# Kernel tuning notes

Hardware: AMD Instinct MI355X
Metric: run time of the kernel (lower is better)

The kernel has to match this reference:

```python
import jax, jax.numpy as jnp
import numpy as np

DIM = 96
HEADS = 6
WS = 8                      # window_size
OWS = int(WS * 0.5) + WS    # overlap_win_size = 12
PAD = (OWS - WS) // 2       # 2
Dd = Hh = Ww = 24
B = 1
L = Dd * Hh * Ww
MLP_H = DIM * 2
TBL = (WS + OWS - 1) ** 3   # 6859 relative-position-bias entries


def setup_inputs() -> dict:
    key = jax.random.key(0)
    ks = jax.random.split(key, 8)
    def n(k, shape, s=0.02):
        return jax.random.normal(k, shape, jnp.float32) * s
    return {
        "x": jax.random.normal(ks[0], (B, L, DIM), jnp.float32),
        "ln1_w": jnp.ones((DIM,), jnp.float32),
        "ln1_b": jnp.zeros((DIM,), jnp.float32),
        "qkv_w": n(ks[1], (3 * DIM, DIM)),
        "qkv_b": jnp.zeros((3 * DIM,), jnp.float32),
        "rpb": n(ks[2], (TBL, HEADS)),
        "proj_w": n(ks[3], (DIM, DIM)),
        "proj_b": jnp.zeros((DIM,), jnp.float32),
        "ln2_w": jnp.ones((DIM,), jnp.float32),
        "ln2_b": jnp.zeros((DIM,), jnp.float32),
        "fc1_w": n(ks[4], (MLP_H, DIM)),
        "fc1_b": jnp.zeros((MLP_H,), jnp.float32),
        "fc2_w": n(ks[5], (DIM, MLP_H)),
        "fc2_b": jnp.zeros((DIM,), jnp.float32),
        "rpi": jax.random.randint(ks[6], (WS ** 3, OWS ** 3), 0, TBL),
        "D": Dd, "H": Hh, "W": Ww,
    }


def _ln(x, w, b):
    m = jnp.mean(x, -1, keepdims=True)
    v = jnp.var(x, -1, keepdims=True)
    return (x - m) / jnp.sqrt(v + 1e-5) * w + b


def _ocab3d(x, ln1_w, ln1_b, qkv_w, qkv_b, rpb, proj_w, proj_b,
            ln2_w, ln2_b, fc1_w, fc1_b, fc2_w, fc2_b, rpi, D, H, W):
    Bz, Lz, C = x.shape
    hd = C // HEADS
    scale = hd ** -0.5
    shortcut = x

    xn = _ln(x, ln1_w, ln1_b).reshape(Bz, D, H, W, C)
    qkv = xn @ qkv_w.T + qkv_b                   # [B,D,H,W,3C]
    q = qkv[..., :C]
    kv = qkv[..., C:]                            # cat(k, v) on channels, [B,D,H,W,2C]

    nD, nH, nW = D // WS, H // WS, W // WS
    nw = nD * nH * nW

    # non-overlapping query windows -> [B*nw, WS^3, C]
    qw = q.reshape(Bz, nD, WS, nH, WS, nW, WS, C)
    qw = qw.transpose(0, 1, 3, 5, 2, 4, 6, 7).reshape(Bz * nw, WS ** 3, C)

    # overlapping kv windows via pad + strided gather (mirrors F.pad + unfold)
    kvp = jnp.pad(kv, ((0, 0), (PAD, PAD), (PAD, PAD), (PAD, PAD), (0, 0)))
    idx_d = (jnp.arange(nD) * WS)[:, None] + jnp.arange(OWS)[None, :]
    idx_h = (jnp.arange(nH) * WS)[:, None] + jnp.arange(OWS)[None, :]
    idx_w = (jnp.arange(nW) * WS)[:, None] + jnp.arange(OWS)[None, :]
    kw = kvp[:, idx_d]                 # [B,nD,OWS,Hp,Wp,2C]
    kw = kw[:, :, :, idx_h]            # [B,nD,OWS,nH,OWS,Wp,2C]
    kw = kw[:, :, :, :, :, idx_w]      # [B,nD,OWS,nH,OWS,nW,OWS,2C]
    kw = kw.transpose(0, 1, 3, 5, 2, 4, 6, 7).reshape(Bz * nw, OWS ** 3, 2 * C)
    kk, vv = kw[..., :C], kw[..., C:]

    qh = qw.reshape(-1, WS ** 3, HEADS, hd).transpose(0, 2, 1, 3) * scale
    kh = kk.reshape(-1, OWS ** 3, HEADS, hd).transpose(0, 2, 1, 3)
    vh = vv.reshape(-1, OWS ** 3, HEADS, hd).transpose(0, 2, 1, 3)

    attn = jnp.einsum('bhqd,bhkd->bhqk', qh, kh)               # [B*nw,H,512,1728]
    bias = rpb[rpi.reshape(-1)].reshape(WS ** 3, OWS ** 3, HEADS).transpose(2, 0, 1)
    attn = jax.nn.softmax(attn + bias[None], axis=-1)
    out = jnp.einsum('bhqk,bhkd->bhqd', attn, vh)
    out = out.transpose(0, 2, 1, 3).reshape(Bz * nw, WS ** 3, C)

    # window reverse -> [B, L, C]
    out = out.reshape(Bz, nD, nH, nW, WS, WS, WS, C)
    out = out.transpose(0, 1, 4, 2, 5, 3, 6, 7).reshape(Bz, D * H * W, C)

    x2 = out @ proj_w.T + proj_b + shortcut
    h1 = jax.nn.gelu(_ln(x2, ln2_w, ln2_b) @ fc1_w.T + fc1_b, approximate=False)
    return x2 + (h1 @ fc2_w.T + fc2_b)


def reference(x, ln1_w, ln1_b, qkv_w, qkv_b, rpb, proj_w, proj_b,
              ln2_w, ln2_b, fc1_w, fc1_b, fc2_w, fc2_b, rpi, D, H, W):
    return _ocab3d(x, ln1_w, ln1_b, qkv_w, qkv_b, rpb, proj_w, proj_b,
                   ln2_w, ln2_b, fc1_w, fc1_b, fc2_w, fc2_b, rpi, D, H, W)
```

## Files before the change

kernel.cpp:

```cpp
#include <hip/hip_runtime.h>
#include <math.h>

#define DIMC   96
#define NHEADS 6
#define HD     16
#define WSZ    8
#define OWSZ   12
#define PADW   2
#define DD     24
#define LTOK   13824
#define NWIN   27
#define NKEY   1728
#define NROW   512
#define MLPH   192
#define PDIM   28
#define PD3    21952
#define TBL    6859
#define LSTR   82944
#define AOSTR  1327104
#define LOG2E  1.4426950408889634f

typedef __attribute__((ext_vector_type(4))) short bf16x4;
typedef __attribute__((ext_vector_type(8))) short bf16x8;
typedef __attribute__((ext_vector_type(4))) float f32x4;

__device__ __forceinline__ unsigned short bfround(float f) {
    unsigned u = __float_as_uint(f);
    return (unsigned short)((u + 0x7FFFu + ((u >> 16) & 1u)) >> 16);
}
__device__ __forceinline__ unsigned bfpack(float a, float b) {
    unsigned ua = __float_as_uint(a), ub = __float_as_uint(b);
    ua = (ua + 0x7FFFu + ((ua >> 16) & 1u)) >> 16;
    ub = (ub + 0x7FFFu + ((ub >> 16) & 1u)) >> 16;
    return ua | (ub << 16);
}
__device__ __forceinline__ uint4 pack8(const float* v) {
    uint4 u;
    u.x = bfpack(v[0], v[1]); u.y = bfpack(v[2], v[3]);
    u.z = bfpack(v[4], v[5]); u.w = bfpack(v[6], v[7]);
    return u;
}
__device__ __forceinline__ bf16x4 pack4(f32x4 p) {
    union { uint2 u; bf16x4 v; } r;
    r.u.x = __builtin_amdgcn_perm(__float_as_uint(p[1]), __float_as_uint(p[0]), 0x07060302u);
    r.u.y = __builtin_amdgcn_perm(__float_as_uint(p[3]), __float_as_uint(p[2]), 0x07060302u);
    return r.v;
}
__device__ __forceinline__ f32x4 cvt4(uint2 b) {
    f32x4 c;
    c[0] = __uint_as_float(b.x << 16);
    c[1] = __uint_as_float(b.x & 0xffff0000u);
    c[2] = __uint_as_float(b.y << 16);
    c[3] = __uint_as_float(b.y & 0xffff0000u);
    return c;
}
__device__ __forceinline__ f32x4 mfma16(bf16x4 a, bf16x4 b, f32x4 c) {
#if __has_builtin(__builtin_amdgcn_mfma_f32_16x16x16bf16_1k)
    return __builtin_amdgcn_mfma_f32_16x16x16bf16_1k(a, b, c, 0, 0, 0);
#else
    bf16x8 a8 = {a[0], a[1], a[2], a[3], 0, 0, 0, 0};
    bf16x8 b8 = {b[0], b[1], b[2], b[3], 0, 0, 0, 0};
    return __builtin_amdgcn_mfma_f32_16x16x32_bf16(a8, b8, c, 0, 0, 0);
#endif
}
__device__ __forceinline__ f32x4 mfma32k(bf16x8 a, bf16x8 b, f32x4 c) {
    return __builtin_amdgcn_mfma_f32_16x16x32_bf16(a, b, c, 0, 0, 0);
}
__device__ __forceinline__ float fexp2(float x) {
#if __has_builtin(__builtin_amdgcn_exp2f)
    return __builtin_amdgcn_exp2f(x);
#else
    return exp2f(x);
#endif
}

#define QKVB 1296
#define ZB   515
#define WPB  45
#define BIASB 216
__global__ __launch_bounds__(256) void qkvz_kernel(
        const float* __restrict__ X, const float* __restrict__ W,
        const float* __restrict__ bias, const float* __restrict__ lnw,
        const float* __restrict__ lnb,
        const float* __restrict__ projw, const float* __restrict__ fc1w,
        const float* __restrict__ fc2w,
        const int* __restrict__ rpi, const float* __restrict__ rpb,
        unsigned short* __restrict__ q16, unsigned short* __restrict__ kvp2,
        uint4* __restrict__ wpack, unsigned short* __restrict__ biasP) {
    __shared__ uint4 Af4[2 * 3 * 4 * 16];
    __shared__ uint4 Bf4[6 * 3 * 4 * 16];
    int bx = blockIdx.x, tid = threadIdx.x;

    if (bx >= QKVB + ZB + WPB) {
        int b2 = bx - (QKVB + ZB + WPB);
        int g = b2 >> 1, qh = b2 & 1;
        int qi = qh * 256 + tid;
        const int* rp = rpi + (long)qi * NKEY + (g >> 2) * 64
                        + ((g >> 1) & 1) * 32 + (g & 1) * 4;
        #pragma unroll
        for (int quadj = 0; quadj < 4; ++quadj) {
            int4 t = *(const int4*)(rp + quadj * 8);
            const float2* p0 = (const float2*)(rpb + (long)t.x * 6);
            const float2* p1 = (const float2*)(rpb + (long)t.y * 6);
            const float2* p2 = (const float2*)(rpb + (long)t.z * 6);
            const float2* p3 = (const float2*)(rpb + (long)t.w * 6);
            unsigned short* oq = biasP + ((long)(g * 4 + quadj) * 512 + qi) * 4;
            #pragma unroll
            for (int hp = 0; hp < 3; ++hp) {
                float2 a0 = p0[hp], a1 = p1[hp], a2 = p2[hp], a3 = p3[hp];
                uint2 ua, ub;
                ua.x = bfpack(a0.x * LOG2E, a1.x * LOG2E);
                ua.y = bfpack(a2.x * LOG2E, a3.x * LOG2E);
                ub.x = bfpack(a0.y * LOG2E, a1.y * LOG2E);
                ub.y = bfpack(a2.y * LOG2E, a3.y * LOG2E);
                *(uint2*)(oq + (long)(hp * 2)     * 884736) = ua;
                *(uint2*)(oq + (long)(hp * 2 + 1) * 884736) = ub;
            }
        }
        return;
    }
    if (bx >= QKVB + ZB) {
        int u = (bx - QKVB - ZB) * 256 + tid;
        if (u < 5760) {
            int p = (u < 1152) ? u : (u < 3456 ? (u - 1152) % 1152 : (u - 3456) % 1152);
            int nn = p & 15, r = p >> 4, qg = r & 3, r2 = r >> 2;
            int kt = r2 % 3, ct = r2 / 3;
            int n = ct * 16 + nn, g = kt * 4 + qg;
            const float* src;
            if (u < 1152)      src = projw + n * 96 + g * 8;
            else if (u < 3456) { int nc = (u - 1152) / 1152; src = fc1w + (long)(nc * 96 + n) * 96 + g * 8; }
            else               { int kh = (u - 3456) / 1152; src = fc2w + (long)n * 192 + kh * 96 + g * 8; }
            const float4* s4 = (const float4*)src;
            float v[8];
            float4 t0 = s4[0], t1 = s4[1];
            v[0]=t0.x; v[1]=t0.y; v[2]=t0.z; v[3]=t0.w;
            v[4]=t1.x; v[5]=t1.y; v[6]=t1.z; v[7]=t1.w;
            wpack[u] = pack8(v);
        }
        return;
    }
    if (bx >= QKVB) {
        int t = (bx - QKVB) * 256 + tid;
        if (t < 21952 * 6) {
            int head = t / PD3, pos = t % PD3;
            int d = pos / 784, h = (pos / 28) % 28, w = pos % 28;
            if (d < 2 || d >= 26 || h < 2 || h >= 26 || w < 2 || w >= 26) {
                uint4* p = (uint4*)(kvp2 + ((long)head * PD3 + pos) * 32);
                uint4 z = make_uint4(0, 0, 0, 0);
                p[0] = z; p[1] = z; p[2] = z; p[3] = z;
            }
        }
        return;
    }

    int nc   = bx % 3;
    int row0 = (bx / 3) * 32;

    if (tid < 128) {
        int row = tid >> 2, part = tid & 3;
        int rt = row >> 4, mm = row & 15;
        float v[24];
        const float4* xp = (const float4*)(X + (long)(row0 + row) * 96 + part * 24);
        float s = 0.f, sq = 0.f;
        #pragma unroll
        for (int i = 0; i < 6; ++i) {
            float4 t = xp[i];
            v[i*4+0] = t.x; v[i*4+1] = t.y; v[i*4+2] = t.z; v[i*4+3] = t.w;
            s  += t.x + t.y + t.z + t.w;
            sq += t.x*t.x + t.y*t.y + t.z*t.z + t.w*t.w;
        }
        s  += __shfl_xor(s, 1);  s  += __shfl_xor(s, 2);
        sq += __shfl_xor(sq, 1); sq += __shfl_xor(sq, 2);
        float mean = s * (1.f / 96.f);
        float inv  = rsqrtf(sq * (1.f / 96.f) - mean * mean + 1e-5f);
        const float4* wp = (const float4*)(lnw + part * 24);
        const float4* bp = (const float4*)(lnb + part * 24);
        #pragma unroll
        for (int i = 0; i < 6; ++i) {
            float4 wv = wp[i], bv = bp[i];
            v[i*4+0] = (v[i*4+0] - mean) * inv * wv.x + bv.x;
            v[i*4+1] = (v[i*4+1] - mean) * inv * wv.y + bv.y;
            v[i*4+2] = (v[i*4+2] - mean) * inv * wv.z + bv.z;
            v[i*4+3] = (v[i*4+3] - mean) * inv * wv.w + bv.w;
        }
        #pragma unroll
        for (int gg = 0; gg < 3; ++gg) {
            int g = part * 3 + gg;
            int kt = g >> 2, qq = g & 3;
            Af4[((rt * 3 + kt) * 4 + qq) * 16 + mm] = pack8(v + gg * 8);
        }
    }
    for (int idx = tid; idx < 96 * 12; idx += 256) {
        int n = idx / 12;
        int g = idx % 12;
        const float4* wp = (const float4*)(W + (long)(nc * 96 + n) * 96 + g * 8);
        float v[8];
        float4 t0 = wp[0], t1 = wp[1];
        v[0]=t0.x; v[1]=t0.y; v[2]=t0.z; v[3]=t0.w;
        v[4]=t1.x; v[5]=t1.y; v[6]=t1.z; v[7]=t1.w;
        int ct = n >> 4, nn = n & 15, kt = g >> 2, qg = g & 3;
        Bf4[((ct * 3 + kt) * 4 + qg) * 16 + nn] = pack8(v);
    }
    __syncthreads();

    int wave = tid >> 6, lane = tid & 63;
    int qq = lane >> 4, mI = lane & 15;
    int rt = wave & 1, cg = wave >> 1;

    f32x4 acc[3];
    #pragma unroll
    for (int j = 0; j < 3; ++j) acc[j] = (f32x4){0.f, 0.f, 0.f, 0.f};
    #pragma unroll
    for (int kt = 0; kt < 3; ++kt) {
        bf16x8 a = *(const bf16x8*)&Af4[((rt * 3 + kt) * 4 + qq) * 16 + mI];
        #pragma unroll
        for (int j = 0; j < 3; ++j) {
            bf16x8 b = *(const bf16x8*)&Bf4[(((cg * 3 + j) * 3 + kt) * 4 + qq) * 16 + mI];
            acc[j] = __builtin_amdgcn_mfma_f32_16x16x32_bf16(a, b, acc[j], 0, 0, 0);
        }
    }

    float bv[3];
    #pragma unroll
    for (int j = 0; j < 3; ++j) bv[j] = bias[nc * 96 + (cg * 3 + j) * 16 + mI];
    #pragma unroll
    for (int r = 0; r < 4; ++r) {
        int row = row0 + rt * 16 + qq * 4 + r;
        if (nc == 0) {
            unsigned short* op = q16 + (long)row * 96;
            #pragma unroll
            for (int j = 0; j < 3; ++j)
                op[(cg * 3 + j) * 16 + mI] = bfround(0.25f * LOG2E * (acc[j][r] + bv[j]));
        } else {
            int d = row / 576, hh = (row / 24) % 24, w2 = row % 24;
            long pos = ((long)(d + 2) * 28 + (hh + 2)) * 28 + (w2 + 2);
            #pragma unroll
            for (int j = 0; j < 3; ++j) {
                int head = cg * 3 + j;
                kvp2[((long)head * PD3 + pos) * 32 +
                     (nc == 2 ? 16 : 0) + mI] = bfround(acc[j][r] + bv[j]);
            }
        }
    }
}

#define KSTR 20
#define VST2 22

#define ATTN_STEP(P, BCUR, BNXT)                                              \
    {                                                                         \
        int c = c0 + cc + (P);                                                \
        bool more = (cc + (P) + 1 < cn);                                      \
        if (more) stgn = *kvaddr(c + 1);                                      \
        __syncthreads();                                                      \
        bf16x4 kf[4];                                                         \
        kf[0] = *(const bf16x4*)&Ks[(P)][kfO];                                \
        kf[1] = *(const bf16x4*)&Ks[(P)][kfO + 4 * KSTR];                     \
        kf[2] = *(const bf16x4*)&Ks[(P)][kfO + 32 * KSTR];                    \
        kf[3] = *(const bf16x4*)&Ks[(P)][kfO + 36 * KSTR];                    \
        f32x4 S[2][4];                                                        \
        _Pragma("unroll")                                                     \
        for (int qt = 0; qt < 2; ++qt) {                                      \
            _Pragma("unroll")                                                 \
            for (int kt = 0; kt < 4; ++kt)                                    \
                S[qt][kt] = mfma16(kf[kt], qf[qt], cvt4(BCUR[qt][kt]));       \
        }                                                                     \
        if (more) {                                                           \
            const unsigned short* bp = bbase + (long)(c + 1) * 32768;         \
            _Pragma("unroll")                                                 \
            for (int qt = 0; qt < 2; ++qt) {                                  \
                _Pragma("unroll")                                             \
                for (int kt = 0; kt < 4; ++kt)                                \
                    BNXT[qt][kt] = *(const uint2*)(bp + kt * 8192 + qt * 64); \
            }                                                                 \
        }                                                                     \
        bf16x8 P8[2][2];                                                      \
        _Pragma("unroll")                                                     \
        for (int qt = 0; qt < 2; ++qt) {                                      \
            _Pragma("unroll")                                                 \
            for (int u = 0; u < 2; ++u) {                                     \
                f32x4 p0, p1;                                                 \
                _Pragma("unroll")                                             \
                for (int r = 0; r < 4; ++r) {                                 \
                    p0[r] = fexp2(S[qt][2 * u][r]);                           \
                    p1[r] = fexp2(S[qt][2 * u + 1][r]);                       \
                }                                                             \
                union { struct { bf16x4 lo, hi; } h; bf16x8 v; } uu;          \
                uu.h.lo = pack4(p0); uu.h.hi = pack4(p1);                     \
                P8[qt][u] = uu.v;                                             \
                lacc[qt] = mfma32k(P8[qt][u], ones8, lacc[qt]);               \
            }                                                                 \
        }                                                                     \
        _Pragma("unroll")                                                     \
        for (int u = 0; u < 2; ++u) {                                         \
            union { unsigned short s[8]; bf16x8 v; } vb;                      \
            int vbase = (u * 32 + quad * 8) * VST2 + m16;                     \
            _Pragma("unroll")                                                 \
            for (int i = 0; i < 8; ++i) vb.s[i] = Vs[(P)][vbase + i * VST2];  \
            o[0] = mfma32k(P8[0][u], vb.v, o[0]);                             \
            o[1] = mfma32k(P8[1][u], vb.v, o[1]);                             \
        }                                                                     \
        if (more) writeLDS((P) ^ 1, stgn);                                    \
    }

__global__ __launch_bounds__(256, 3) void attn_kernel(
        const unsigned short* __restrict__ q, const unsigned short* __restrict__ kvp2,
        const unsigned short* __restrict__ biasP, float* __restrict__ ao,
        float* __restrict__ lbuf) {
    __shared__ unsigned short Ks[2][64 * KSTR];
    __shared__ unsigned short Vs[2][64 * VST2];
    int bid = blockIdx.x;
    int w = bid / 48, rem = bid % 48;
    int head = rem >> 3;
    int quart = (rem >> 1) & 3, half = rem & 1;
    int wd8 = (w / 9) * 8, wh8 = ((w / 3) % 3) * 8, ww8 = (w % 3) * 8;
    int tid = threadIdx.x, wave = tid >> 6, lane = tid & 63;
    int quad = lane >> 4, m16 = lane & 15;
    int key = tid >> 2, part = tid & 3;
    int c0 = half ? 13 : 0;
    int cn = half ? 14 : 13;

    auto kvaddr = [&](int c) -> const uint4* {
        int jg = c * 64 + key;
        int i = jg / 144, jh = (jg / 12) % 12, jw = jg % 12;
        long sp = ((long)(wd8 + i) * PDIM + (wh8 + jh)) * PDIM + (ww8 + jw);
        return (const uint4*)(kvp2 + ((long)head * PD3 + sp) * 32 + part * 8);
    };
    auto writeLDS = [&](int b, uint4 v) {
        if (part < 2) {
            *(uint2*)(&Ks[b][key * KSTR + part * 8])     = make_uint2(v.x, v.y);
            *(uint2*)(&Ks[b][key * KSTR + part * 8 + 4]) = make_uint2(v.z, v.w);
        } else {
            int d0 = (part - 2) * 8;
            *(uint2*)(&Vs[b][key * VST2 + d0])     = make_uint2(v.x, v.y);
            *(uint2*)(&Vs[b][key * VST2 + d0 + 4]) = make_uint2(v.z, v.w);
        }
    };

    bf16x4 qf[2];
    #pragma unroll
    for (int qt = 0; qt < 2; ++qt) {
        int ql = quart * 128 + wave * 32 + qt * 16 + m16;
        int ld = ql >> 6, lh = (ql >> 3) & 7, lw = ql & 7;
        int g = ((wd8 + ld) * 24 + (wh8 + lh)) * 24 + (ww8 + lw);
        qf[qt] = *(const bf16x4*)(q + (long)g * 96 + head * 16 + quad * 4);
    }

    const unsigned short* bbase = biasP + (long)head * 884736 + quad * 2048
                         + ((quart * 128 + wave * 32 + m16) << 2);
    uint2 bb0[2][4], bb1[2][4];
    #pragma unroll
    for (int qt = 0; qt < 2; ++qt)
        #pragma unroll
        for (int kt = 0; kt < 4; ++kt)
            bb0[qt][kt] = *(const uint2*)(bbase + (long)(c0 * 4 + kt) * 8192 + qt * 64);

    writeLDS(0, *kvaddr(c0));

    int kfO = ((m16 >> 2) * 8 + (m16 & 3)) * KSTR + quad * 4;

    const bf16x8 ones8 = {(short)0x3F80, (short)0x3F80, (short)0x3F80, (short)0x3F80,
                          (short)0x3F80, (short)0x3F80, (short)0x3F80, (short)0x3F80};
    f32x4 o[2], lacc[2];
    o[0] = (f32x4){0.f,0.f,0.f,0.f}; o[1] = (f32x4){0.f,0.f,0.f,0.f};
    lacc[0] = o[0]; lacc[1] = o[1];
    uint4 stgn;

    for (int cc = 0; cc < cn; cc += 2) {
        ATTN_STEP(0, bb0, bb1)
        if (cc + 1 < cn) ATTN_STEP(1, bb1, bb0)
    }

    float* aout = ao + (long)half * AOSTR;
    float* lout = lbuf + (long)half * LSTR;
    #pragma unroll
    for (int qt = 0; qt < 2; ++qt) {
        #pragma unroll
        for (int r = 0; r < 4; ++r) {
            int ql = quart * 128 + wave * 32 + qt * 16 + quad * 4 + r;
            int ld = ql >> 6, lh = (ql >> 3) & 7, lw = ql & 7;
            int g = ((wd8 + ld) * 24 + (wh8 + lh)) * 24 + (ww8 + lw);
            aout[(long)g * 96 + head * 16 + m16] = o[qt][r];
            if (m16 == 0) lout[g * 6 + head] = lacc[qt][r];
        }
    }
}

#define X2S 100
__global__ __launch_bounds__(512) void mlp_kernel(
        const float* __restrict__ ao0, const float* __restrict__ ao1,
        const float* __restrict__ lbuf, const uint4* __restrict__ wpack,
        const float* __restrict__ projb, const float* __restrict__ x,
        const float* __restrict__ ln2w, const float* __restrict__ ln2b,
        const float* __restrict__ fc1b, const float* __restrict__ fc2b,
        float* __restrict__ out) {
    __shared__ uint4 Ws[5760];
    __shared__ uint4 Af4[4 * 3 * 4 * 16];
    __shared__ float x2s[64 * X2S];
    __shared__ unsigned short h16[64 * 192];
    int tid = threadIdx.x;
    int row0 = blockIdx.x * 64;
    int wave = tid >> 6, lane = tid & 63;
    int qq = lane >> 4, mI = lane & 15;
    int rt = wave & 3, cg = wave >> 2;

    for (int idx = tid; idx < 5760; idx += 512) Ws[idx] = wpack[idx];

    if (tid < 256) {
        int row = tid >> 2, part = tid & 3;
        int rtA = row >> 4, mm = row & 15;
        int grow = row0 + row;
        const float4* a0 = (const float4*)(ao0 + (long)grow * 96 + part * 24);
        const float4* a1 = (const float4*)(ao1 + (long)grow * 96 + part * 24);
        int ha = (part * 3) >> 1, hb = ha + 1;
        float inva = 1.f / (lbuf[grow*6 + ha] + lbuf[LSTR + grow*6 + ha]);
        float invb = 1.f / (lbuf[grow*6 + hb] + lbuf[LSTR + grow*6 + hb]);
        float v[24];
        #pragma unroll
        for (int i = 0; i < 6; ++i) {
            float4 u0 = a0[i], u1 = a1[i];
            #pragma unroll
            for (int j = 0; j < 4; ++j) {
                int gc = part * 24 + i * 4 + j;
                float lv = ((gc >> 4) == ha) ? inva : invb;
                float s = (j==0?u0.x+u1.x : j==1?u0.y+u1.y : j==2?u0.z+u1.z : u0.w+u1.w);
                v[i*4+j] = s * lv;
            }
        }
        #pragma unroll
        for (int gg = 0; gg < 3; ++gg) {
            int g = part * 3 + gg;
            int kt = g >> 2, q4 = g & 3;
            Af4[((rtA * 3 + kt) * 4 + q4) * 16 + mm] = pack8(v + gg * 8);
        }
    }
    __syncthreads();

    {
        f32x4 acc[3];
        #pragma unroll
        for (int j = 0; j < 3; ++j) acc[j] = (f32x4){0.f,0.f,0.f,0.f};
        #pragma unroll
        for (int kt = 0; kt < 3; ++kt) {
            bf16x8 a = *(const bf16x8*)&Af4[((rt * 3 + kt) * 4 + qq) * 16 + mI];
            #pragma unroll
            for (int j = 0; j < 3; ++j) {
                bf16x8 b = *(const bf16x8*)&Ws[(((cg * 3 + j) * 3 + kt) * 4 + qq) * 16 + mI];
                acc[j] = __builtin_amdgcn_mfma_f32_16x16x32_bf16(a, b, acc[j], 0, 0, 0);
            }
        }
        float bv[3];
        #pragma unroll
        for (int j = 0; j < 3; ++j) bv[j] = projb[(cg * 3 + j) * 16 + mI];
        #pragma unroll
        for (int r = 0; r < 4; ++r) {
            int row = rt * 16 + qq * 4 + r;
            int grow = row0 + row;
            #pragma unroll
            for (int j = 0; j < 3; ++j) {
                int col = (cg * 3 + j) * 16 + mI;
                x2s[row * X2S + col] = acc[j][r] + bv[j] + x[(long)grow * 96 + col];
            }
        }
    }
    __syncthreads();

    if (tid < 256) {
        int row = tid >> 2, part = tid & 3;
        int rtA = row >> 4, mm = row & 15;
        float v[24];
        const float4* xp = (const float4*)(x2s + row * X2S + part * 24);
        float s = 0.f, sq = 0.f;
        #pragma unroll
        for (int i = 0; i < 6; ++i) {
            float4 t = xp[i];
            v[i*4+0] = t.x; v[i*4+1] = t.y; v[i*4+2] = t.z; v[i*4+3] = t.w;
            s  += t.x + t.y + t.z + t.w;
            sq += t.x*t.x + t.y*t.y + t.z*t.z + t.w*t.w;
        }
        s  += __shfl_xor(s, 1);  s  += __shfl_xor(s, 2);
        sq += __shfl_xor(sq, 1); sq += __shfl_xor(sq, 2);
        float mean = s * (1.f / 96.f);
        float inv  = rsqrtf(sq * (1.f / 96.f) - mean * mean + 1e-5f);
        const float4* wp = (const float4*)(ln2w + part * 24);
        const float4* bp = (const float4*)(ln2b + part * 24);
        #pragma unroll
        for (int i = 0; i < 6; ++i) {
            float4 wv = wp[i], bv = bp[i];
            v[i*4+0] = (v[i*4+0] - mean) * inv * wv.x + bv.x;
            v[i*4+1] = (v[i*4+1] - mean) * inv * wv.y + bv.y;
            v[i*4+2] = (v[i*4+2] - mean) * inv * wv.z + bv.z;
            v[i*4+3] = (v[i*4+3] - mean) * inv * wv.w + bv.w;
        }
        #pragma unroll
        for (int gg = 0; gg < 3; ++gg) {
            int g = part * 3 + gg;
            int kt = g >> 2, q4 = g & 3;
            Af4[((rtA * 3 + kt) * 4 + q4) * 16 + mm] = pack8(v + gg * 8);
        }
    }
    __syncthreads();

    #pragma unroll
    for (int nc = 0; nc < 2; ++nc) {
        f32x4 acc[3];
        #pragma unroll
        for (int j = 0; j < 3; ++j) acc[j] = (f32x4){0.f,0.f,0.f,0.f};
        #pragma unroll
        for (int kt = 0; kt < 3; ++kt) {
            bf16x8 a = *(const bf16x8*)&Af4[((rt * 3 + kt) * 4 + qq) * 16 + mI];
            #pragma unroll
            for (int j = 0; j < 3; ++j) {
                bf16x8 b = *(const bf16x8*)&Ws[1152 + nc * 1152 +
                               (((cg * 3 + j) * 3 + kt) * 4 + qq) * 16 + mI];
                acc[j] = __builtin_amdgcn_mfma_f32_16x16x32_bf16(a, b, acc[j], 0, 0, 0);
            }
        }
        float bv[3];
        #pragma unroll
        for (int j = 0; j < 3; ++j) bv[j] = fc1b[nc * 96 + (cg * 3 + j) * 16 + mI];
        #pragma unroll
        for (int r = 0; r < 4; ++r) {
            int row = rt * 16 + qq * 4 + r;
            #pragma unroll
            for (int j = 0; j < 3; ++j) {
                int col = nc * 96 + (cg * 3 + j) * 16 + mI;
                float v = acc[j][r] + bv[j];
                float g = 0.5f * v * (1.f + erff(v * 0.70710678f));
                int fi = (((row >> 4) * 6 + (col >> 5)) * 4 + ((col >> 3) & 3)) * 16 + (row & 15);
                h16[fi * 8 + (col & 7)] = bfround(g);
            }
        }
    }
    __syncthreads();

    f32x4 acc2[3];
    #pragma unroll
    for (int j = 0; j < 3; ++j) acc2[j] = (f32x4){0.f,0.f,0.f,0.f};
    #pragma unroll
    for (int kh = 0; kh < 2; ++kh) {
        #pragma unroll
        for (int kt = 0; kt < 3; ++kt) {
            int ktA = kh * 3 + kt;
            bf16x8 a = *(const bf16x8*)&h16[(((rt * 6 + ktA) * 4 + qq) * 16 + mI) * 8];
            #pragma unroll
            for (int j = 0; j < 3; ++j) {
                bf16x8 b = *(const bf16x8*)&Ws[3456 + kh * 1152 +
                               (((cg * 3 + j) * 3 + kt) * 4 + qq) * 16 + mI];
                acc2[j] = __builtin_amdgcn_mfma_f32_16x16x32_bf16(a, b, acc2[j], 0, 0, 0);
            }
        }
    }
    float bv[3];
    #pragma unroll
    for (int j = 0; j < 3; ++j) bv[j] = fc2b[(cg * 3 + j) * 16 + mI];
    #pragma unroll
    for (int r = 0; r < 4; ++r) {
        int row = rt * 16 + qq * 4 + r;
        int grow = row0 + row;
        #pragma unroll
        for (int j = 0; j < 3; ++j) {
            int col = (cg * 3 + j) * 16 + mI;
            out[(long)grow * 96 + col] = acc2[j][r] + bv[j] + x2s[row * X2S + col];
        }
    }
}

extern "C" void kernel_launch(void* const* d_in, const int* in_sizes, int n_in,
                              void* d_out, int out_size, void* d_ws, size_t ws_size,
                              hipStream_t stream) {
    const float* x     = (const float*)d_in[0];
    const float* ln1w  = (const float*)d_in[1];
    const float* ln1b  = (const float*)d_in[2];
    const float* qkvw  = (const float*)d_in[3];
    const float* qkvb  = (const float*)d_in[4];
    const float* rpb   = (const float*)d_in[5];
    const float* projw = (const float*)d_in[6];
    const float* projb = (const float*)d_in[7];
    const float* ln2w  = (const float*)d_in[8];
    const float* ln2b  = (const float*)d_in[9];
    const float* fc1w  = (const float*)d_in[10];
    const float* fc1b  = (const float*)d_in[11];
    const float* fc2w  = (const float*)d_in[12];
    const float* fc2b  = (const float*)d_in[13];
    const int*   rpi   = (const int*)d_in[14];
    float* outp = (float*)d_out;

    float* ws = (float*)d_ws;
    float*          aop    = ws;
    unsigned short* q16    = (unsigned short*)(ws + 2654208);
    unsigned short* kvp16  = (unsigned short*)(ws + 3317760);
    unsigned short* biasPh = (unsigned short*)(ws + 5425152);
    float*          lbuf   = ws + 10733568;
    uint4*          wpack  = (uint4*)(ws + 10899456);

    qkvz_kernel<<<QKVB + ZB + WPB + BIASB, 256, 0, stream>>>(
        x, qkvw, qkvb, ln1w, ln1b, projw, fc1w, fc2w, rpi, rpb,
        q16, kvp16, wpack, biasPh);
    attn_kernel<<<NWIN * NHEADS * 4 * 2, 256, 0, stream>>>(q16, kvp16, biasPh, aop, lbuf);
    mlp_kernel<<<LTOK / 64, 512, 0, stream>>>(aop, aop + AOSTR, lbuf, wpack, projb, x,
                                              ln2w, ln2b, fc1b, fc2b, outp);
}
```

Measured before the change: 162.5 us.

## Stage attention bias tiles into LDS via async global-to-LDS loads

```diff
diff --git a/kernel.cpp b/kernel.cpp
--- a/kernel.cpp
+++ b/kernel.cpp
@@ -73,6 +73,15 @@
     return exp2f(x);
 #endif
 }
+__device__ __forceinline__ void gload16(const unsigned short* g, unsigned short* l, int lane) {
+#if __has_builtin(__builtin_amdgcn_global_load_lds)
+    __builtin_amdgcn_global_load_lds(
+        (const __attribute__((address_space(1))) void*)g,
+        (__attribute__((address_space(3))) void*)l, 16, 0, 0);
+#else
+    *((uint4*)l + lane) = *(const uint4*)(g + (long)lane * 8);
+#endif
+}
 
 #define QKVB 1296
 #define ZB   515
@@ -93,18 +102,21 @@
 
     if (bx >= QKVB + ZB + WPB) {
         int b2 = bx - (QKVB + ZB + WPB);
-        int g = b2 >> 1, qh = b2 & 1;
-        int qi = qh * 256 + tid;
-        const int* rp = rpi + (long)qi * NKEY + (g >> 2) * 64
-                        + ((g >> 1) & 1) * 32 + (g & 1) * 4;
-        #pragma unroll
-        for (int quadj = 0; quadj < 4; ++quadj) {
-            int4 t = *(const int4*)(rp + quadj * 8);
+        int c  = b2 % 27;
+        int qp = b2 / 27;
+        int quart = qp >> 1, qt = qp & 1;
+        int wavep = tid >> 6, m16p = tid & 15, quadp = (tid >> 4) & 3;
+        int q = quart * 128 + wavep * 32 + qt * 16 + m16p;
+        const int* rp = rpi + (long)q * NKEY + c * 64 + quadp * 8;
+        long obase = (long)quart * 221184 + c * 8192 + qt * 4096 + tid * 4;
+        #pragma unroll
+        for (int kt = 0; kt < 4; ++kt) {
+            int4 t = *(const int4*)(rp + (kt >> 1) * 32 + (kt & 1) * 4);
             const float2* p0 = (const float2*)(rpb + (long)t.x * 6);
             const float2* p1 = (const float2*)(rpb + (long)t.y * 6);
             const float2* p2 = (const float2*)(rpb + (long)t.z * 6);
             const float2* p3 = (const float2*)(rpb + (long)t.w * 6);
-            unsigned short* oq = biasP + ((long)(g * 4 + quadj) * 512 + qi) * 4;
+            unsigned short* oq = biasP + obase + kt * 1024;
             #pragma unroll
             for (int hp = 0; hp < 3; ++hp) {
                 float2 a0 = p0[hp], a1 = p1[hp], a2 = p2[hp], a3 = p3[hp];
@@ -113,7 +125,7 @@
                 ua.y = bfpack(a2.x * LOG2E, a3.x * LOG2E);
                 ub.x = bfpack(a0.y * LOG2E, a1.y * LOG2E);
                 ub.y = bfpack(a2.y * LOG2E, a3.y * LOG2E);
-                *(uint2*)(oq + (long)(hp * 2)     * 884736) = ua;
+                *(uint2*)(oq + (long)(hp * 2) * 884736)     = ua;
                 *(uint2*)(oq + (long)(hp * 2 + 1) * 884736) = ub;
             }
         }
@@ -244,46 +256,42 @@
     }
 }
 
-#define KSTR 20
 #define VST2 22
 
-#define ATTN_STEP(P, BCUR, BNXT)                                              \
+#define ATTN_STEP(P)                                                          \
     {                                                                         \
         int c = c0 + cc + (P);                                                \
         bool more = (cc + (P) + 1 < cn);                                      \
-        if (more) stgn = *kvaddr(c + 1);                                      \
         __syncthreads();                                                      \
+        if (more) {                                                           \
+            const unsigned short* bsrc = btile + (long)(c + 1) * 8192;        \
+            _Pragma("unroll")                                                 \
+            for (int i = 0; i < 4; ++i)                                       \
+                gload16(bsrc + ((i * 4 + wave) * 64 + lane) * 8,              \
+                        &biasL[(P) ^ 1][(i * 4 + wave) * 512], lane);         \
+            stgn = *kvaddr(c + 1);                                            \
+        }                                                                     \
         bf16x4 kf[4];                                                         \
         kf[0] = *(const bf16x4*)&Ks[(P)][kfO];                                \
-        kf[1] = *(const bf16x4*)&Ks[(P)][kfO + 4 * KSTR];                     \
-        kf[2] = *(const bf16x4*)&Ks[(P)][kfO + 32 * KSTR];                    \
-        kf[3] = *(const bf16x4*)&Ks[(P)][kfO + 36 * KSTR];                    \
-        f32x4 S[2][4];                                                        \
-        _Pragma("unroll")                                                     \
-        for (int qt = 0; qt < 2; ++qt) {                                      \
-            _Pragma("unroll")                                                 \
-            for (int kt = 0; kt < 4; ++kt)                                    \
-                S[qt][kt] = mfma16(kf[kt], qf[qt], cvt4(BCUR[qt][kt]));       \
-        }                                                                     \
-        if (more) {                                                           \
-            const unsigned short* bp = bbase + (long)(c + 1) * 32768;         \
-            _Pragma("unroll")                                                 \
-            for (int qt = 0; qt < 2; ++qt) {                                  \
-                _Pragma("unroll")                                             \
-                for (int kt = 0; kt < 4; ++kt)                                \
-                    BNXT[qt][kt] = *(const uint2*)(bp + kt * 8192 + qt * 64); \
-            }                                                                 \
-        }                                                                     \
+        kf[1] = *(const bf16x4*)&Ks[(P)][kfO + 64];                           \
+        kf[2] = *(const bf16x4*)&Ks[(P)][kfO + 512];                          \
+        kf[3] = *(const bf16x4*)&Ks[(P)][kfO + 576];                          \
         bf16x8 P8[2][2];                                                      \
         _Pragma("unroll")                                                     \
         for (int qt = 0; qt < 2; ++qt) {                                      \
+            f32x4 S[4];                                                       \
+            _Pragma("unroll")                                                 \
+            for (int kt = 0; kt < 4; ++kt) {                                  \
+                uint2 bb = *(const uint2*)&biasL[(P)][(qt * 4 + kt) * 1024 + tid * 4]; \
+                S[kt] = mfma16(kf[kt], qf[qt], cvt4(bb));                     \
+            }                                                                 \
             _Pragma("unroll")                                                 \
             for (int u = 0; u < 2; ++u) {                                     \
                 f32x4 p0, p1;                                                 \
                 _Pragma("unroll")                                             \
                 for (int r = 0; r < 4; ++r) {                                 \
-                    p0[r] = fexp2(S[qt][2 * u][r]);                           \
-                    p1[r] = fexp2(S[qt][2 * u + 1][r]);                       \
+                    p0[r] = fexp2(S[2 * u][r]);                               \
+                    p1[r] = fexp2(S[2 * u + 1][r]);                           \
                 }                                                             \
                 union { struct { bf16x4 lo, hi; } h; bf16x8 v; } uu;          \
                 uu.h.lo = pack4(p0); uu.h.hi = pack4(p1);                     \
@@ -307,8 +315,9 @@
         const unsigned short* __restrict__ q, const unsigned short* __restrict__ kvp2,
         const unsigned short* __restrict__ biasP, float* __restrict__ ao,
         float* __restrict__ lbuf) {
-    __shared__ unsigned short Ks[2][64 * KSTR];
+    __shared__ unsigned short Ks[2][64 * 16];
     __shared__ unsigned short Vs[2][64 * VST2];
+    __shared__ unsigned short biasL[2][8192];
     int bid = blockIdx.x;
     int w = bid / 48, rem = bid % 48;
     int head = rem >> 3;
@@ -328,8 +337,10 @@
     };
     auto writeLDS = [&](int b, uint4 v) {
         if (part < 2) {
-            *(uint2*)(&Ks[b][key * KSTR + part * 8])     = make_uint2(v.x, v.y);
-            *(uint2*)(&Ks[b][key * KSTR + part * 8 + 4]) = make_uint2(v.z, v.w);
+            int swz0 = ((2 * part)     ^ (key & 3)) * 4;
+            int swz1 = ((2 * part + 1) ^ (key & 3)) * 4;
+            *(uint2*)(&Ks[b][key * 16 + swz0]) = make_uint2(v.x, v.y);
+            *(uint2*)(&Ks[b][key * 16 + swz1]) = make_uint2(v.z, v.w);
         } else {
             int d0 = (part - 2) * 8;
             *(uint2*)(&Vs[b][key * VST2 + d0])     = make_uint2(v.x, v.y);
@@ -346,18 +357,18 @@
         qf[qt] = *(const bf16x4*)(q + (long)g * 96 + head * 16 + quad * 4);
     }
 
-    const unsigned short* bbase = biasP + (long)head * 884736 + quad * 2048
-                         + ((quart * 128 + wave * 32 + m16) << 2);
-    uint2 bb0[2][4], bb1[2][4];
-    #pragma unroll
-    for (int qt = 0; qt < 2; ++qt)
-        #pragma unroll
-        for (int kt = 0; kt < 4; ++kt)
-            bb0[qt][kt] = *(const uint2*)(bbase + (long)(c0 * 4 + kt) * 8192 + qt * 64);
-
-    writeLDS(0, *kvaddr(c0));
-
-    int kfO = ((m16 >> 2) * 8 + (m16 & 3)) * KSTR + quad * 4;
+    const unsigned short* btile = biasP + (long)head * 884736 + (long)quart * 221184;
+
+    {
+        const unsigned short* bsrc = btile + (long)c0 * 8192;
+        #pragma unroll
+        for (int i = 0; i < 4; ++i)
+            gload16(bsrc + ((i * 4 + wave) * 64 + lane) * 8,
+                    &biasL[0][(i * 4 + wave) * 512], lane);
+        writeLDS(0, *kvaddr(c0));
+    }
+
+    int kfO = ((m16 >> 2) * 8 + (m16 & 3)) * 16 + ((quad ^ (m16 & 3)) * 4);
 
     const bf16x8 ones8 = {(short)0x3F80, (short)0x3F80, (short)0x3F80, (short)0x3F80,
                           (short)0x3F80, (short)0x3F80, (short)0x3F80, (short)0x3F80};
@@ -366,9 +377,10 @@
     lacc[0] = o[0]; lacc[1] = o[1];
     uint4 stgn;
 
+    #pragma unroll 1
     for (int cc = 0; cc < cn; cc += 2) {
-        ATTN_STEP(0, bb0, bb1)
-        if (cc + 1 < cn) ATTN_STEP(1, bb1, bb0)
+        ATTN_STEP(0)
+        if (cc + 1 < cn) ATTN_STEP(1)
     }
 
     float* aout = ao + (long)half * AOSTR;
```

After: 171.4 us. 1.05x slower.

## Relayout bias buffer per thread and transpose V in LDS for vector reads

Applied to the files above, without the earlier changes.

```diff
diff --git a/kernel.cpp b/kernel.cpp
--- a/kernel.cpp
+++ b/kernel.cpp
@@ -93,18 +93,19 @@
 
     if (bx >= QKVB + ZB + WPB) {
         int b2 = bx - (QKVB + ZB + WPB);
-        int g = b2 >> 1, qh = b2 & 1;
-        int qi = qh * 256 + tid;
-        const int* rp = rpi + (long)qi * NKEY + (g >> 2) * 64
-                        + ((g >> 1) & 1) * 32 + (g & 1) * 4;
-        #pragma unroll
-        for (int quadj = 0; quadj < 4; ++quadj) {
-            int4 t = *(const int4*)(rp + quadj * 8);
+        int c  = b2 % 27;
+        int qp = b2 / 27;
+        int quart = qp >> 1, qt = qp & 1;
+        int wavep = tid >> 6, quadp = (tid >> 4) & 3, m16p = tid & 15;
+        int q = quart * 128 + wavep * 32 + qt * 16 + m16p;
+        const int* rp = rpi + (long)q * NKEY + c * 64 + quadp * 8;
+        #pragma unroll
+        for (int kt = 0; kt < 4; ++kt) {
+            int4 t = *(const int4*)(rp + (kt >> 1) * 32 + (kt & 1) * 4);
             const float2* p0 = (const float2*)(rpb + (long)t.x * 6);
             const float2* p1 = (const float2*)(rpb + (long)t.y * 6);
             const float2* p2 = (const float2*)(rpb + (long)t.z * 6);
             const float2* p3 = (const float2*)(rpb + (long)t.w * 6);
-            unsigned short* oq = biasP + ((long)(g * 4 + quadj) * 512 + qi) * 4;
             #pragma unroll
             for (int hp = 0; hp < 3; ++hp) {
                 float2 a0 = p0[hp], a1 = p1[hp], a2 = p2[hp], a3 = p3[hp];
@@ -113,8 +114,10 @@
                 ua.y = bfpack(a2.x * LOG2E, a3.x * LOG2E);
                 ub.x = bfpack(a0.y * LOG2E, a1.y * LOG2E);
                 ub.y = bfpack(a2.y * LOG2E, a3.y * LOG2E);
-                *(uint2*)(oq + (long)(hp * 2)     * 884736) = ua;
-                *(uint2*)(oq + (long)(hp * 2 + 1) * 884736) = ub;
+                *(uint2*)(biasP + ((long)((2*hp)   * 4 + quart) * 27 + c) * 8192
+                          + qt * 4096 + tid * 16 + kt * 4) = ua;
+                *(uint2*)(biasP + ((long)((2*hp+1) * 4 + quart) * 27 + c) * 8192
+                          + qt * 4096 + tid * 16 + kt * 4) = ub;
             }
         }
         return;
@@ -245,33 +248,37 @@
 }
 
 #define KSTR 20
-#define VST2 22
+#define VKP  66
 
 #define ATTN_STEP(P, BCUR, BNXT)                                              \
     {                                                                         \
-        int c = c0 + cc + (P);                                                \
         bool more = (cc + (P) + 1 < cn);                                      \
-        if (more) stgn = *kvaddr(c + 1);                                      \
+        if (more) stgn = *kvaddr(c0 + cc + (P) + 1);                          \
         __syncthreads();                                                      \
         bf16x4 kf[4];                                                         \
-        kf[0] = *(const bf16x4*)&Ks[(P)][kfO];                                \
-        kf[1] = *(const bf16x4*)&Ks[(P)][kfO + 4 * KSTR];                     \
-        kf[2] = *(const bf16x4*)&Ks[(P)][kfO + 32 * KSTR];                    \
-        kf[3] = *(const bf16x4*)&Ks[(P)][kfO + 36 * KSTR];                    \
+        _Pragma("unroll")                                                     \
+        for (int kt = 0; kt < 4; ++kt)                                        \
+            kf[kt] = *(const bf16x4*)&Ks[(P)][(kt * 16 + m16) * KSTR + quad * 4]; \
+        bf16x8 vb0 = *(const bf16x8*)&Vt[(P)][m16 * VKP + quad * 8];          \
+        bf16x8 vb1 = *(const bf16x8*)&Vt[(P)][m16 * VKP + 32 + quad * 8];     \
         f32x4 S[2][4];                                                        \
         _Pragma("unroll")                                                     \
         for (int qt = 0; qt < 2; ++qt) {                                      \
             _Pragma("unroll")                                                 \
-            for (int kt = 0; kt < 4; ++kt)                                    \
-                S[qt][kt] = mfma16(kf[kt], qf[qt], cvt4(BCUR[qt][kt]));       \
+            for (int kt = 0; kt < 4; ++kt) {                                  \
+                uint4 bj = BCUR[qt][kt >> 1];                                 \
+                uint2 bb = (kt & 1) ? make_uint2(bj.z, bj.w)                  \
+                                    : make_uint2(bj.x, bj.y);                 \
+                S[qt][kt] = mfma16(kf[kt], qf[qt], cvt4(bb));                 \
+            }                                                                 \
         }                                                                     \
         if (more) {                                                           \
-            const unsigned short* bp = bbase + (long)(c + 1) * 32768;         \
+            const unsigned short* bp = bbase + (long)(c0 + cc + (P) + 1) * 8192 \
+                                       + tid * 16;                            \
             _Pragma("unroll")                                                 \
             for (int qt = 0; qt < 2; ++qt) {                                  \
-                _Pragma("unroll")                                             \
-                for (int kt = 0; kt < 4; ++kt)                                \
-                    BNXT[qt][kt] = *(const uint2*)(bp + kt * 8192 + qt * 64); \
+                BNXT[qt][0] = *(const uint4*)(bp + qt * 4096);                \
+                BNXT[qt][1] = *(const uint4*)(bp + qt * 4096 + 8);            \
             }                                                                 \
         }                                                                     \
         bf16x8 P8[2][2];                                                      \
@@ -291,15 +298,10 @@
                 lacc[qt] = mfma32k(P8[qt][u], ones8, lacc[qt]);               \
             }                                                                 \
         }                                                                     \
-        _Pragma("unroll")                                                     \
-        for (int u = 0; u < 2; ++u) {                                         \
-            union { unsigned short s[8]; bf16x8 v; } vb;                      \
-            int vbase = (u * 32 + quad * 8) * VST2 + m16;                     \
-            _Pragma("unroll")                                                 \
-            for (int i = 0; i < 8; ++i) vb.s[i] = Vs[(P)][vbase + i * VST2];  \
-            o[0] = mfma32k(P8[0][u], vb.v, o[0]);                             \
-            o[1] = mfma32k(P8[1][u], vb.v, o[1]);                             \
-        }                                                                     \
+        o[0] = mfma32k(P8[0][0], vb0, o[0]);                                  \
+        o[1] = mfma32k(P8[1][0], vb0, o[1]);                                  \
+        o[0] = mfma32k(P8[0][1], vb1, o[0]);                                  \
+        o[1] = mfma32k(P8[1][1], vb1, o[1]);                                  \
         if (more) writeLDS((P) ^ 1, stgn);                                    \
     }
 
@@ -308,7 +310,7 @@
         const unsigned short* __restrict__ biasP, float* __restrict__ ao,
         float* __restrict__ lbuf) {
     __shared__ unsigned short Ks[2][64 * KSTR];
-    __shared__ unsigned short Vs[2][64 * VST2];
+    __shared__ unsigned short Vt[2][16 * VKP];
     int bid = blockIdx.x;
     int w = bid / 48, rem = bid % 48;
     int head = rem >> 3;
@@ -320,6 +322,8 @@
     int c0 = half ? 13 : 0;
     int cn = half ? 14 : 13;
 
+    int skey = (key & 35) | ((key & 4) << 2) | ((key >> 1) & 12);
+
     auto kvaddr = [&](int c) -> const uint4* {
         int jg = c * 64 + key;
         int i = jg / 144, jh = (jg / 12) % 12, jw = jg % 12;
@@ -328,12 +332,19 @@
     };
     auto writeLDS = [&](int b, uint4 v) {
         if (part < 2) {
-            *(uint2*)(&Ks[b][key * KSTR + part * 8])     = make_uint2(v.x, v.y);
-            *(uint2*)(&Ks[b][key * KSTR + part * 8 + 4]) = make_uint2(v.z, v.w);
+            *(uint2*)(&Ks[b][skey * KSTR + part * 8])     = make_uint2(v.x, v.y);
+            *(uint2*)(&Ks[b][skey * KSTR + part * 8 + 4]) = make_uint2(v.z, v.w);
         } else {
             int d0 = (part - 2) * 8;
-            *(uint2*)(&Vs[b][key * VST2 + d0])     = make_uint2(v.x, v.y);
-            *(uint2*)(&Vs[b][key * VST2 + d0 + 4]) = make_uint2(v.z, v.w);
+            unsigned short* vp = &Vt[b][d0 * VKP + key];
+            vp[0 * VKP] = (unsigned short)(v.x);
+            vp[1 * VKP] = (unsigned short)(v.x >> 16);
+            vp[2 * VKP] = (unsigned short)(v.y);
+            vp[3 * VKP] = (unsigned short)(v.y >> 16);
+            vp[4 * VKP] = (unsigned short)(v.z);
+            vp[5 * VKP] = (unsigned short)(v.z >> 16);
+            vp[6 * VKP] = (unsigned short)(v.w);
+            vp[7 * VKP] = (unsigned short)(v.w >> 16);
         }
     };
 
@@ -346,18 +357,18 @@
         qf[qt] = *(const bf16x4*)(q + (long)g * 96 + head * 16 + quad * 4);
     }
 
-    const unsigned short* bbase = biasP + (long)head * 884736 + quad * 2048
-                         + ((quart * 128 + wave * 32 + m16) << 2);
-    uint2 bb0[2][4], bb1[2][4];
-    #pragma unroll
-    for (int qt = 0; qt < 2; ++qt)
-        #pragma unroll
-        for (int kt = 0; kt < 4; ++kt)
-            bb0[qt][kt] = *(const uint2*)(bbase + (long)(c0 * 4 + kt) * 8192 + qt * 64);
+    const unsigned short* bbase = biasP + ((long)(head * 4 + quart) * 27) * 8192;
+    uint4 bb0[2][2], bb1[2][2];
+    {
+        const unsigned short* bp = bbase + (long)c0 * 8192 + tid * 16;
+        #pragma unroll
+        for (int qt = 0; qt < 2; ++qt) {
+            bb0[qt][0] = *(const uint4*)(bp + qt * 4096);
+            bb0[qt][1] = *(const uint4*)(bp + qt * 4096 + 8);
+        }
+    }
 
     writeLDS(0, *kvaddr(c0));
-
-    int kfO = ((m16 >> 2) * 8 + (m16 & 3)) * KSTR + quad * 4;
 
     const bf16x8 ones8 = {(short)0x3F80, (short)0x3F80, (short)0x3F80, (short)0x3F80,
                           (short)0x3F80, (short)0x3F80, (short)0x3F80, (short)0x3F80};
```

New measurement: 158.8 us. -2.2%, faster.
